# Kernel tuning notes

Measured on AMD Instinct MI355X. Metric: run time of the kernel, lower is better.

## Reference

```python
import jax, jax.numpy as jnp
import numpy as np

N = 1024   # num nodes
D = 128    # feat_dim (input_dim)


def setup_inputs() -> dict:
    key = jax.random.key(0)
    k1, k2 = jax.random.split(key)
    x = jax.random.normal(k1, (N, D), dtype=jnp.float32)
    # nn.Linear(D, 1) -> weight vector [D], bias [1] (xavier init weight, zero bias)
    w_vec = jax.random.normal(k2, (D,), dtype=jnp.float32) * np.sqrt(2.0 / (D + 1))
    w_bias = jnp.zeros((1,), dtype=jnp.float32)
    return {"x": x, "w_vec": w_vec, "w_bias": w_bias}


def reference(x, w_vec, w_bias):
    # diff[i, j, d] = |x[i, d] - x[j, d]|  (repeat_interleave row-major -> x[i] minus broadcast x[j])
    diff = jnp.abs(x[:, None, :] - x[None, :, :])          # [N, N, D]
    scores = jnp.einsum('ijd,d->ij', diff, w_vec) + w_bias[0]  # Linear(D,1) -> [N, N]
    scores = jax.nn.relu(scores)
    return jax.nn.softmax(scores, axis=1)
```

## Files before the change

kernel.cpp:

```cpp
#include <hip/hip_runtime.h>

#define N 1024
#define D 128
#define PAD 132

__global__ __launch_bounds__(1024, 4) void scores_kernel(
    const float* __restrict__ x, const float* __restrict__ w,
    const float* __restrict__ bias, float* __restrict__ E,
    float* __restrict__ part) {
  __shared__ float smem[2 * 64 * PAD];
  float* sxi = smem;
  float* sxj = smem + 64 * PAD;

  const int t  = threadIdx.x;
  const int bi = blockIdx.y * 64;
  const int bj = blockIdx.x * 64;

  {
    const int c  = t & 31;
    const int r0 = t >> 5;
    #pragma unroll
    for (int p = 0; p < 2; ++p) {
      const int r = r0 + p * 32;
      const float4 vi = reinterpret_cast<const float4*>(x)[(bi + r) * 32 + c];
      *reinterpret_cast<float4*>(&sxi[r * PAD + c * 4]) = vi;
      const float4 vj = reinterpret_cast<const float4*>(x)[(bj + r) * 32 + c];
      *reinterpret_cast<float4*>(&sxj[r * PAD + c * 4]) = vj;
    }
  }
  __syncthreads();

  const int g  = __builtin_amdgcn_readfirstlane(t >> 8);
  const int s  = t & 255;
  const int tx = s & 15;
  const int ty = s >> 4;
  const int d0 = g * 32;

  float acc[4][4];
  #pragma unroll
  for (int a = 0; a < 4; ++a)
    #pragma unroll
    for (int b = 0; b < 4; ++b) acc[a][b] = 0.f;

  #pragma unroll 2
  for (int dc = 0; dc < 8; ++dc) {
    const float4 W = reinterpret_cast<const float4*>(w)[(d0 >> 2) + dc];
    const int d = d0 + dc * 4;
    float4 A[4], B[4];
    #pragma unroll
    for (int a = 0; a < 4; ++a)
      A[a] = *reinterpret_cast<const float4*>(&sxi[(ty + 16 * a) * PAD + d]);
    #pragma unroll
    for (int b = 0; b < 4; ++b)
      B[b] = *reinterpret_cast<const float4*>(&sxj[(tx + 16 * b) * PAD + d]);

    #pragma unroll
    for (int a = 0; a < 4; ++a) {
      #pragma unroll
      for (int b = 0; b < 4; ++b) {
        float v = acc[a][b];
        v = fmaf(fabsf(A[a].x - B[b].x), W.x, v);
        v = fmaf(fabsf(A[a].y - B[b].y), W.y, v);
        v = fmaf(fabsf(A[a].z - B[b].z), W.z, v);
        v = fmaf(fabsf(A[a].w - B[b].w), W.w, v);
        acc[a][b] = v;
      }
    }
  }
  __syncthreads();

  float* comb = smem;
  if (g > 0) {
    float* dst = comb + ((g - 1) * 256 + s) * 17;
    #pragma unroll
    for (int k = 0; k < 16; ++k) dst[k] = acc[k >> 2][k & 3];
  }
  __syncthreads();

  if (g == 0) {
    #pragma unroll
    for (int q = 0; q < 3; ++q) {
      const float* src = comb + (q * 256 + s) * 17;
      #pragma unroll
      for (int k = 0; k < 16; ++k) acc[k >> 2][k & 3] += src[k];
    }

    const float bv = bias[0];
    #pragma unroll
    for (int a = 0; a < 4; ++a) {
      float p = 0.f;
      #pragma unroll
      for (int b = 0; b < 4; ++b) {
        const float ev = __expf(fmaxf(acc[a][b] + bv, 0.f));
        acc[a][b] = ev;
        p += ev;
      }
      #pragma unroll
      for (int o = 1; o < 16; o <<= 1) p += __shfl_xor(p, o, 64);
      if (tx == 0) part[(bi + ty + 16 * a) * 16 + blockIdx.x] = p;
    }

    #pragma unroll
    for (int a = 0; a < 4; ++a) {
      const int row = bi + ty + 16 * a;
      #pragma unroll
      for (int b = 0; b < 4; ++b)
        E[row * N + bj + tx + 16 * b] = acc[a][b];
    }
  }
}

__global__ __launch_bounds__(256) void scale_kernel(
    float* __restrict__ S, const float* __restrict__ part) {
  const int row = blockIdx.x;
  const int t   = threadIdx.x;

  float p = part[row * 16 + (t & 15)];
  #pragma unroll
  for (int o = 1; o < 16; o <<= 1) p += __shfl_xor(p, o, 64);
  const float r = 1.0f / p;

  float4* rowp = reinterpret_cast<float4*>(S + row * N);
  float4 v = rowp[t];
  v.x *= r; v.y *= r; v.z *= r; v.w *= r;
  rowp[t] = v;
}

extern "C" void kernel_launch(void* const* d_in, const int* in_sizes, int n_in,
                              void* d_out, int out_size, void* d_ws, size_t ws_size,
                              hipStream_t stream) {
  const float* x = (const float*)d_in[0];
  const float* w = (const float*)d_in[1];
  const float* b = (const float*)d_in[2];
  float* out  = (float*)d_out;
  float* part = (float*)d_ws;

  dim3 grid(N / 64, N / 64);
  scores_kernel<<<grid, 1024, 0, stream>>>(x, w, b, out, part);
  scale_kernel<<<N, 256, 0, stream>>>(out, part);
}
```

Measured before the change: 75.26 us.

## Shrink score tile to 64x32 with 512-thread blocks and 2-way d-split

```diff
diff --git a/kernel.cpp b/kernel.cpp
--- a/kernel.cpp
+++ b/kernel.cpp
@@ -4,29 +4,36 @@
 #define D 128
 #define PAD 132
 
-__global__ __launch_bounds__(1024, 4) void scores_kernel(
+__global__ __launch_bounds__(512, 4) void scores_kernel(
     const float* __restrict__ x, const float* __restrict__ w,
     const float* __restrict__ bias, float* __restrict__ E,
     float* __restrict__ part) {
-  __shared__ float smem[2 * 64 * PAD];
-  float* sxi = smem;
-  float* sxj = smem + 64 * PAD;
+  __shared__ float sxi[64 * PAD];
+  __shared__ float sxj[32 * PAD];
+  __shared__ float sw[D];
 
   const int t  = threadIdx.x;
   const int bi = blockIdx.y * 64;
-  const int bj = blockIdx.x * 64;
+  const int bj = blockIdx.x * 32;
 
   {
     const int c  = t & 31;
     const int r0 = t >> 5;
     #pragma unroll
+    for (int p = 0; p < 4; ++p) {
+      const int r = r0 + p * 16;
+      const float4 v = reinterpret_cast<const float4*>(x)[(bi + r) * 32 + c];
+      *reinterpret_cast<float4*>(&sxi[r * PAD + c * 4]) = v;
+    }
+    #pragma unroll
     for (int p = 0; p < 2; ++p) {
-      const int r = r0 + p * 32;
-      const float4 vi = reinterpret_cast<const float4*>(x)[(bi + r) * 32 + c];
-      *reinterpret_cast<float4*>(&sxi[r * PAD + c * 4]) = vi;
-      const float4 vj = reinterpret_cast<const float4*>(x)[(bj + r) * 32 + c];
-      *reinterpret_cast<float4*>(&sxj[r * PAD + c * 4]) = vj;
+      const int r = r0 + p * 16;
+      const float4 v = reinterpret_cast<const float4*>(x)[(bj + r) * 32 + c];
+      *reinterpret_cast<float4*>(&sxj[r * PAD + c * 4]) = v;
     }
+    if (t < 32)
+      *reinterpret_cast<float4*>(&sw[t * 4]) =
+          reinterpret_cast<const float4*>(w)[t];
   }
   __syncthreads();
 
@@ -34,30 +41,30 @@
   const int s  = t & 255;
   const int tx = s & 15;
   const int ty = s >> 4;
-  const int d0 = g * 32;
+  const int d0 = g * 64;
 
-  float acc[4][4];
+  float acc[4][2];
   #pragma unroll
   for (int a = 0; a < 4; ++a)
     #pragma unroll
-    for (int b = 0; b < 4; ++b) acc[a][b] = 0.f;
+    for (int b = 0; b < 2; ++b) acc[a][b] = 0.f;
 
-  #pragma unroll 2
-  for (int dc = 0; dc < 8; ++dc) {
-    const float4 W = reinterpret_cast<const float4*>(w)[(d0 >> 2) + dc];
+  #pragma unroll 4
+  for (int dc = 0; dc < 16; ++dc) {
     const int d = d0 + dc * 4;
-    float4 A[4], B[4];
+    const float4 W = *reinterpret_cast<const float4*>(&sw[d]);
+    float4 A[4], B[2];
     #pragma unroll
     for (int a = 0; a < 4; ++a)
       A[a] = *reinterpret_cast<const float4*>(&sxi[(ty + 16 * a) * PAD + d]);
     #pragma unroll
-    for (int b = 0; b < 4; ++b)
+    for (int b = 0; b < 2; ++b)
       B[b] = *reinterpret_cast<const float4*>(&sxj[(tx + 16 * b) * PAD + d]);
 
     #pragma unroll
     for (int a = 0; a < 4; ++a) {
       #pragma unroll
-      for (int b = 0; b < 4; ++b) {
+      for (int b = 0; b < 2; ++b) {
         float v = acc[a][b];
         v = fmaf(fabsf(A[a].x - B[b].x), W.x, v);
         v = fmaf(fabsf(A[a].y - B[b].y), W.y, v);
@@ -69,42 +76,39 @@
   }
   __syncthreads();
 
-  float* comb = smem;
-  if (g > 0) {
-    float* dst = comb + ((g - 1) * 256 + s) * 17;
+  float* comb = sxi;
+  if (g == 1) {
+    float* dst = comb + s * 9;
     #pragma unroll
-    for (int k = 0; k < 16; ++k) dst[k] = acc[k >> 2][k & 3];
+    for (int k = 0; k < 8; ++k) dst[k] = acc[k >> 1][k & 1];
   }
   __syncthreads();
 
   if (g == 0) {
+    const float* src = comb + s * 9;
     #pragma unroll
-    for (int q = 0; q < 3; ++q) {
-      const float* src = comb + (q * 256 + s) * 17;
-      #pragma unroll
-      for (int k = 0; k < 16; ++k) acc[k >> 2][k & 3] += src[k];
-    }
+    for (int k = 0; k < 8; ++k) acc[k >> 1][k & 1] += src[k];
 
     const float bv = bias[0];
     #pragma unroll
     for (int a = 0; a < 4; ++a) {
       float p = 0.f;
       #pragma unroll
-      for (int b = 0; b < 4; ++b) {
+      for (int b = 0; b < 2; ++b) {
         const float ev = __expf(fmaxf(acc[a][b] + bv, 0.f));
         acc[a][b] = ev;
         p += ev;
       }
       #pragma unroll
       for (int o = 1; o < 16; o <<= 1) p += __shfl_xor(p, o, 64);
-      if (tx == 0) part[(bi + ty + 16 * a) * 16 + blockIdx.x] = p;
+      if (tx == 0) part[(bi + ty + 16 * a) * 32 + blockIdx.x] = p;
     }
 
     #pragma unroll
     for (int a = 0; a < 4; ++a) {
       const int row = bi + ty + 16 * a;
       #pragma unroll
-      for (int b = 0; b < 4; ++b)
+      for (int b = 0; b < 2; ++b)
         E[row * N + bj + tx + 16 * b] = acc[a][b];
     }
   }
@@ -115,9 +119,9 @@
   const int row = blockIdx.x;
   const int t   = threadIdx.x;
 
-  float p = part[row * 16 + (t & 15)];
+  float p = part[row * 32 + (t & 31)];
   #pragma unroll
-  for (int o = 1; o < 16; o <<= 1) p += __shfl_xor(p, o, 64);
+  for (int o = 1; o < 32; o <<= 1) p += __shfl_xor(p, o, 64);
   const float r = 1.0f / p;
 
   float4* rowp = reinterpret_cast<float4*>(S + row * N);
@@ -135,7 +139,7 @@
   float* out  = (float*)d_out;
   float* part = (float*)d_ws;
 
-  dim3 grid(N / 64, N / 64);
-  scores_kernel<<<grid, 1024, 0, stream>>>(x, w, b, out, part);
+  dim3 grid(N / 32, N / 64);
+  scores_kernel<<<grid, 512, 0, stream>>>(x, w, b, out, part);
   scale_kernel<<<N, 256, 0, stream>>>(out, part);
 }
```

Measured after the change: 72.83 us. 1.03x faster.
